# Kernel tuning notes

Measured on AMD Instinct MI355X. Metric: run time of the kernel, lower is better.

The kernel has to match this reference:

```python
import jax, jax.numpy as jnp
import numpy as np
from jax import lax

T, IN, H, B = 256, 2048, 2048, 8
K_INIT = 4.0

def setup_inputs() -> dict:
    key = jax.random.key(0)
    k1, k2, k3, k4, k5, k6 = jax.random.split(key, 6)
    k = 1.0 / np.sqrt(H)
    # simplex-init alphas: off-diagonal -K, diagonal log(1-(B-1)exp(-K)), plus small noise
    base = jnp.full((B, B), -K_INIT) + jnp.eye(B) * (np.log(1.0 - (B - 1) * np.exp(-K_INIT)) + K_INIT)
    alphas = base + 0.01 * jax.random.normal(k1, (B, B))
    return {
        "x": jax.random.normal(k2, (T, IN), dtype=jnp.float32),            # sentence of word vectors
        "W": jax.random.uniform(k3, (B, H, H), minval=-k, maxval=k),       # B recurrent basis matrices
        "alphas": alphas.astype(jnp.float32),                               # [B, B] mixing logits
        "bias": jax.random.uniform(k4, (H,), minval=-k, maxval=k),
        "v": jnp.eye(H, IN, dtype=jnp.float32),                             # input projection (init = eye)
        "fc_w": jax.random.uniform(k5, (H, H), minval=-k, maxval=k),
        "fc_b": jax.random.uniform(k6, (H,), minval=-k, maxval=k),
        "alpha_int": 0,
    }

def reference(x, W, alphas, bias, v, fc_w, fc_b, alpha_int):
    # normalise_alpha == softmax over the selected alpha row (simplex=True)
    alpha = jax.nn.softmax(alphas[alpha_int])                 # [B]
    u = jnp.einsum('b,bij->ij', alpha, W)                     # mixed recurrent weight [H, H]
    igates = x @ v.T                                          # all input gates at once [T, H]

    def step(h, ig):                                          # Elman cell: h = tanh(v@w + u@h + bias)
        h = jnp.tanh(ig + u @ h + bias)
        return h, None

    h0 = jnp.zeros((H,), dtype=x.dtype)
    h, _ = lax.scan(step, h0, igates)                         # sequential over T words
    out = jax.nn.sigmoid(h @ fc_w.T + fc_b)                   # fc(hidden.t()) then sigmoid
    return out[None, :]                                       # [1, H]
```

## Files before the change

kernel.cpp:

```cpp
#include <hip/hip_runtime.h>
#include <math.h>

#define HDIM    2048
#define TSTEPS  256
#define BBASIS  8
#define RING_D  4
#define NR      8

typedef float f32x4 __attribute__((ext_vector_type(4)));

__device__ inline void store_coherent_f4(float* p, f32x4 v) {
    asm volatile("global_store_dwordx4 %0, %1, off sc0 sc1"
                 :: "v"(p), "v"(v) : "memory");
}
__device__ inline f32x4 load_coherent_f4(const float* p) {
    f32x4 a;
    asm volatile("global_load_dwordx4 %0, %1, off sc0 sc1\n\t"
                 "s_waitcnt vmcnt(0)"
                 : "=&v"(a) : "v"(p) : "memory");
    return a;
}

__global__ __launch_bounds__(256, 1)
void prep_kernel(const float* __restrict__ x,
                 const float* __restrict__ W,
                 const float* __restrict__ alphas,
                 const float* __restrict__ v,
                 const int*   __restrict__ alpha_int,
                 float*       __restrict__ u_g,
                 float*       __restrict__ ig_g)
{
    const int tid  = threadIdx.x;
    const int bid  = blockIdx.x;
    const int wave = tid >> 6;
    const int lane = tid & 63;
    const int r0   = bid * 8 + wave * 2;

    __shared__ __align__(16) float x_tile[8][HDIM];

    const int ai = alpha_int[0];
    float a[BBASIS];
    float mx = -1e30f;
    #pragma unroll
    for (int b = 0; b < BBASIS; ++b) { a[b] = alphas[ai * BBASIS + b]; mx = fmaxf(mx, a[b]); }
    float ssum = 0.f;
    #pragma unroll
    for (int b = 0; b < BBASIS; ++b) { a[b] = expf(a[b] - mx); ssum += a[b]; }
    const float inv_s = 1.f / ssum;

    {
        float acc[2][8][4];
        #pragma unroll
        for (int q = 0; q < 2; ++q)
            #pragma unroll
            for (int k = 0; k < 8; ++k)
                #pragma unroll
                for (int i = 0; i < 4; ++i) acc[q][k][i] = 0.f;

        for (int b = 0; b < BBASIS; ++b) {
            const float ab = a[b] * inv_s;
            #pragma unroll
            for (int q = 0; q < 2; ++q) {
                const f32x4* wrow = (const f32x4*)(W + ((size_t)b * HDIM + (size_t)(r0 + q)) * HDIM);
                #pragma unroll
                for (int k = 0; k < 8; ++k) {
                    f32x4 w4 = wrow[lane + 64 * k];
                    acc[q][k][0] += ab * w4.x;
                    acc[q][k][1] += ab * w4.y;
                    acc[q][k][2] += ab * w4.z;
                    acc[q][k][3] += ab * w4.w;
                }
            }
        }
        #pragma unroll
        for (int q = 0; q < 2; ++q) {
            f32x4* urow = (f32x4*)(u_g + (size_t)(r0 + q) * HDIM);
            #pragma unroll
            for (int k = 0; k < 8; ++k) {
                f32x4 w4;
                w4.x = acc[q][k][0]; w4.y = acc[q][k][1];
                w4.z = acc[q][k][2]; w4.w = acc[q][k][3];
                urow[lane + 64 * k] = w4;
            }
        }
    }

    {
        float vr[2][8][4];
        #pragma unroll
        for (int q = 0; q < 2; ++q) {
            const f32x4* vrow = (const f32x4*)(v + (size_t)(r0 + q) * HDIM);
            #pragma unroll
            for (int k = 0; k < 8; ++k) {
                f32x4 t4 = vrow[lane + 64 * k];
                vr[q][k][0] = t4.x; vr[q][k][1] = t4.y; vr[q][k][2] = t4.z; vr[q][k][3] = t4.w;
            }
        }
        for (int tb = 0; tb < TSTEPS; tb += 8) {
            #pragma unroll
            for (int j = 0; j < 8; ++j) {
                const f32x4* xt4 = (const f32x4*)(x + (size_t)(tb + j) * HDIM);
                #pragma unroll
                for (int c = 0; c < 2; ++c)
                    ((f32x4*)x_tile[j])[tid + 256 * c] = xt4[tid + 256 * c];
            }
            __syncthreads();
            #pragma unroll
            for (int j = 0; j < 8; ++j) {
                float acc0 = 0.f, acc1 = 0.f;
                #pragma unroll
                for (int k = 0; k < 8; ++k) {
                    const f32x4 x4 = ((const f32x4*)x_tile[j])[lane + 64 * k];
                    acc0 += vr[0][k][0]*x4.x + vr[0][k][1]*x4.y + vr[0][k][2]*x4.z + vr[0][k][3]*x4.w;
                    acc1 += vr[1][k][0]*x4.x + vr[1][k][1]*x4.y + vr[1][k][2]*x4.z + vr[1][k][3]*x4.w;
                }
                #pragma unroll
                for (int off = 32; off > 0; off >>= 1) {
                    acc0 += __shfl_xor(acc0, off, 64);
                    acc1 += __shfl_xor(acc1, off, 64);
                }
                if (lane == 0)
                    *(float2*)&ig_g[(size_t)(tb + j) * HDIM + r0] = make_float2(acc0, acc1);
            }
            __syncthreads();
        }
    }
}

__global__ __launch_bounds__(512, 2)
void scan_kernel(const float* __restrict__ bias,
                 const float* __restrict__ fc_w,
                 const float* __restrict__ fc_b,
                 float*       __restrict__ out,
                 const float* __restrict__ u_g,
                 const float* __restrict__ ig_g,
                 float*       __restrict__ ring)
{
    const int tid  = threadIdx.x;
    const int bid  = blockIdx.x;
    const int wave = tid >> 6;
    const int lane = tid & 63;
    const int r0   = bid * 32 + wave * 4;

    __shared__ __align__(16) float h_lds[2][HDIM];
    __shared__ __align__(16) float ig_lds[TSTEPS][32];

    #pragma unroll
    for (int i = 0; i < 4; ++i) {
        const int c  = tid + 512 * i;
        const int t  = c >> 3;
        const int ch = c & 7;
        f32x4 g = *(const f32x4*)&ig_g[(size_t)t * HDIM + bid * 32 + ch * 4];
        *(f32x4*)&ig_lds[t][ch * 4] = g;
    }

    f32x4 U[4][8];
    #pragma unroll
    for (int q = 0; q < 4; ++q) {
        const float* urow = u_g + (size_t)(r0 + q) * HDIM;
        #pragma unroll
        for (int k = 0; k < 8; ++k) {
            asm volatile("global_load_dwordx4 %0, %1, off"
                         : "=&v"(U[q][k])
                         : "v"(urow + (size_t)(lane + 64 * k) * 4));
        }
    }
    asm volatile("s_waitcnt vmcnt(0)" ::: "memory");
    __builtin_amdgcn_sched_barrier(0);

    float bias4[4];
    #pragma unroll
    for (int q = 0; q < 4; ++q) bias4[q] = bias[r0 + q];

    h_lds[0][tid]        = 0.f;
    h_lds[0][tid + 512]  = 0.f;
    h_lds[0][tid + 1024] = 0.f;
    h_lds[0][tid + 1536] = 0.f;
    __syncthreads();

    int cur = 0;
    for (int t = 0; t < TSTEPS; ++t) {
        float acc0 = 0.f, acc1 = 0.f, acc2 = 0.f, acc3 = 0.f;
        #pragma unroll
        for (int k = 0; k < 8; ++k) {
            const f32x4 h4 = ((const f32x4*)h_lds[cur])[lane + 64 * k];
            acc0 += U[0][k].x*h4.x + U[0][k].y*h4.y + U[0][k].z*h4.z + U[0][k].w*h4.w;
            acc1 += U[1][k].x*h4.x + U[1][k].y*h4.y + U[1][k].z*h4.z + U[1][k].w*h4.w;
            acc2 += U[2][k].x*h4.x + U[2][k].y*h4.y + U[2][k].z*h4.z + U[2][k].w*h4.w;
            acc3 += U[3][k].x*h4.x + U[3][k].y*h4.y + U[3][k].z*h4.z + U[3][k].w*h4.w;
        }
        #pragma unroll
        for (int off = 32; off > 0; off >>= 1) {
            acc0 += __shfl_xor(acc0, off, 64);
            acc1 += __shfl_xor(acc1, off, 64);
            acc2 += __shfl_xor(acc2, off, 64);
            acc3 += __shfl_xor(acc3, off, 64);
        }
        const int   st     = t + 1;
        const float bias_f = ((st >> 2) & 1) ? 8.0f : -8.0f;
        float* slotbase = ring + (size_t)((st & (RING_D - 1)) * NR) * HDIM;

        const f32x4 ig4 = *(const f32x4*)&ig_lds[t][wave * 4];
        f32x4 hv;
        hv.x = tanhf(acc0 + ig4.x + bias4[0]) + bias_f;
        hv.y = tanhf(acc1 + ig4.y + bias4[1]) + bias_f;
        hv.z = tanhf(acc2 + ig4.z + bias4[2]) + bias_f;
        hv.w = tanhf(acc3 + ig4.w + bias4[3]) + bias_f;
        if (lane < NR)
            store_coherent_f4(slotbase + (size_t)lane * HDIM + r0, hv);

        const float* pp = slotbase + (size_t)(bid & (NR - 1)) * HDIM + 4 * tid;
        f32x4 hq = load_coherent_f4(pp);
        if (bias_f > 0.0f) {
            while (!((hq.x > 6.5f) & (hq.y > 6.5f) & (hq.z > 6.5f) & (hq.w > 6.5f))) {
                __builtin_amdgcn_s_sleep(1);
                hq = load_coherent_f4(pp);
            }
        } else {
            while (!((hq.x < -6.5f) & (hq.y < -6.5f) & (hq.z < -6.5f) & (hq.w < -6.5f))) {
                __builtin_amdgcn_s_sleep(1);
                hq = load_coherent_f4(pp);
            }
        }
        hq.x -= bias_f; hq.y -= bias_f; hq.z -= bias_f; hq.w -= bias_f;

        const int nxt = cur ^ 1;
        *(f32x4*)&h_lds[nxt][4 * tid] = hq;
        __syncthreads();
        cur = nxt;
    }

    {
        float acc0 = 0.f, acc1 = 0.f, acc2 = 0.f, acc3 = 0.f;
        const f32x4* f0 = (const f32x4*)(fc_w + (size_t)(r0 + 0) * HDIM);
        const f32x4* f1 = (const f32x4*)(fc_w + (size_t)(r0 + 1) * HDIM);
        const f32x4* f2 = (const f32x4*)(fc_w + (size_t)(r0 + 2) * HDIM);
        const f32x4* f3 = (const f32x4*)(fc_w + (size_t)(r0 + 3) * HDIM);
        #pragma unroll
        for (int k = 0; k < 8; ++k) {
            const f32x4 h4 = ((const f32x4*)h_lds[cur])[lane + 64 * k];
            f32x4 w0 = f0[lane + 64 * k];
            f32x4 w1 = f1[lane + 64 * k];
            f32x4 w2 = f2[lane + 64 * k];
            f32x4 w3 = f3[lane + 64 * k];
            acc0 += w0.x*h4.x + w0.y*h4.y + w0.z*h4.z + w0.w*h4.w;
            acc1 += w1.x*h4.x + w1.y*h4.y + w1.z*h4.z + w1.w*h4.w;
            acc2 += w2.x*h4.x + w2.y*h4.y + w2.z*h4.z + w2.w*h4.w;
            acc3 += w3.x*h4.x + w3.y*h4.y + w3.z*h4.z + w3.w*h4.w;
        }
        #pragma unroll
        for (int off = 32; off > 0; off >>= 1) {
            acc0 += __shfl_xor(acc0, off, 64);
            acc1 += __shfl_xor(acc1, off, 64);
            acc2 += __shfl_xor(acc2, off, 64);
            acc3 += __shfl_xor(acc3, off, 64);
        }
        if (lane == 0) {
            f32x4 o4;
            o4.x = 1.f / (1.f + expf(-(acc0 + fc_b[r0 + 0])));
            o4.y = 1.f / (1.f + expf(-(acc1 + fc_b[r0 + 1])));
            o4.z = 1.f / (1.f + expf(-(acc2 + fc_b[r0 + 2])));
            o4.w = 1.f / (1.f + expf(-(acc3 + fc_b[r0 + 3])));
            *(f32x4*)&out[r0] = o4;
        }
    }
}

__global__ __launch_bounds__(512, 1)
void elman_scan_self(const float* __restrict__ x,
                     const float* __restrict__ W,
                     const float* __restrict__ alphas,
                     const float* __restrict__ bias,
                     const float* __restrict__ v,
                     const float* __restrict__ fc_w,
                     const float* __restrict__ fc_b,
                     const int*   __restrict__ alpha_int,
                     float*       __restrict__ out,
                     float*       __restrict__ hbuf)
{
    const int tid  = threadIdx.x;
    const int bid  = blockIdx.x;
    const int wave = tid >> 6;
    const int lane = tid & 63;
    const int r0   = bid * 32 + wave * 4;

    __shared__ __align__(16) float x_tile[8][HDIM];
    __shared__ __align__(16) float ig_lds[TSTEPS][32];
    __shared__ __align__(16) float h_lds[2][HDIM];

    const int ai = alpha_int[0];
    float a[BBASIS];
    float mx = -1e30f;
    #pragma unroll
    for (int b = 0; b < BBASIS; ++b) { a[b] = alphas[ai * BBASIS + b]; mx = fmaxf(mx, a[b]); }
    float ssum = 0.f;
    #pragma unroll
    for (int b = 0; b < BBASIS; ++b) { a[b] = expf(a[b] - mx); ssum += a[b]; }
    const float inv_s = 1.f / ssum;

    {
        float vr[4][8][4];
        #pragma unroll
        for (int q = 0; q < 4; ++q) {
            const f32x4* vrow = (const f32x4*)(v + (size_t)(r0 + q) * HDIM);
            #pragma unroll
            for (int k = 0; k < 8; ++k) {
                f32x4 t4 = vrow[lane + 64 * k];
                vr[q][k][0] = t4.x; vr[q][k][1] = t4.y; vr[q][k][2] = t4.z; vr[q][k][3] = t4.w;
            }
        }
        for (int tb = 0; tb < TSTEPS; tb += 8) {
            #pragma unroll
            for (int j = 0; j < 8; ++j)
                *(f32x4*)&x_tile[j][4 * tid] =
                    *(const f32x4*)&x[(size_t)(tb + j) * HDIM + 4 * tid];
            __syncthreads();
            #pragma unroll
            for (int j = 0; j < 8; ++j) {
                float acc0 = 0.f, acc1 = 0.f, acc2 = 0.f, acc3 = 0.f;
                #pragma unroll
                for (int k = 0; k < 8; ++k) {
                    const f32x4 x4 = ((const f32x4*)x_tile[j])[lane + 64 * k];
                    acc0 += vr[0][k][0]*x4.x + vr[0][k][1]*x4.y + vr[0][k][2]*x4.z + vr[0][k][3]*x4.w;
                    acc1 += vr[1][k][0]*x4.x + vr[1][k][1]*x4.y + vr[1][k][2]*x4.z + vr[1][k][3]*x4.w;
                    acc2 += vr[2][k][0]*x4.x + vr[2][k][1]*x4.y + vr[2][k][2]*x4.z + vr[2][k][3]*x4.w;
                    acc3 += vr[3][k][0]*x4.x + vr[3][k][1]*x4.y + vr[3][k][2]*x4.z + vr[3][k][3]*x4.w;
                }
                #pragma unroll
                for (int off = 32; off > 0; off >>= 1) {
                    acc0 += __shfl_xor(acc0, off, 64);
                    acc1 += __shfl_xor(acc1, off, 64);
                    acc2 += __shfl_xor(acc2, off, 64);
                    acc3 += __shfl_xor(acc3, off, 64);
                }
                if (lane == 0) {
                    f32x4 ig4; ig4.x = acc0; ig4.y = acc1; ig4.z = acc2; ig4.w = acc3;
                    *(f32x4*)&ig_lds[tb + j][wave * 4] = ig4;
                }
            }
            __syncthreads();
        }
    }

    float u_reg[4][8][4];
    #pragma unroll
    for (int q = 0; q < 4; ++q)
        #pragma unroll
        for (int k = 0; k < 8; ++k)
            #pragma unroll
            for (int i = 0; i < 4; ++i) u_reg[q][k][i] = 0.f;

    for (int b = 0; b < BBASIS; ++b) {
        const float ab = a[b] * inv_s;
        #pragma unroll
        for (int q = 0; q < 4; ++q) {
            const f32x4* wrow = (const f32x4*)(W + ((size_t)b * HDIM + (size_t)(r0 + q)) * HDIM);
            #pragma unroll
            for (int k = 0; k < 8; ++k) {
                f32x4 w4 = wrow[lane + 64 * k];
                u_reg[q][k][0] += ab * w4.x;
                u_reg[q][k][1] += ab * w4.y;
                u_reg[q][k][2] += ab * w4.z;
                u_reg[q][k][3] += ab * w4.w;
            }
        }
    }
    float bias4[4];
    #pragma unroll
    for (int q = 0; q < 4; ++q) bias4[q] = bias[r0 + q];

    h_lds[0][tid] = 0.f; h_lds[0][tid + 512] = 0.f;
    h_lds[0][tid + 1024] = 0.f; h_lds[0][tid + 1536] = 0.f;
    __syncthreads();

    int cur = 0;
    for (int t = 0; t < TSTEPS; ++t) {
        float acc0 = 0.f, acc1 = 0.f, acc2 = 0.f, acc3 = 0.f;
        #pragma unroll
        for (int k = 0; k < 8; ++k) {
            const f32x4 h4 = ((const f32x4*)h_lds[cur])[lane + 64 * k];
            acc0 += u_reg[0][k][0]*h4.x + u_reg[0][k][1]*h4.y + u_reg[0][k][2]*h4.z + u_reg[0][k][3]*h4.w;
            acc1 += u_reg[1][k][0]*h4.x + u_reg[1][k][1]*h4.y + u_reg[1][k][2]*h4.z + u_reg[1][k][3]*h4.w;
            acc2 += u_reg[2][k][0]*h4.x + u_reg[2][k][1]*h4.y + u_reg[2][k][2]*h4.z + u_reg[2][k][3]*h4.w;
            acc3 += u_reg[3][k][0]*h4.x + u_reg[3][k][1]*h4.y + u_reg[3][k][2]*h4.z + u_reg[3][k][3]*h4.w;
        }
        #pragma unroll
        for (int off = 32; off > 0; off >>= 1) {
            acc0 += __shfl_xor(acc0, off, 64);
            acc1 += __shfl_xor(acc1, off, 64);
            acc2 += __shfl_xor(acc2, off, 64);
            acc3 += __shfl_xor(acc3, off, 64);
        }
        float* hg = hbuf + (size_t)(t + 1) * HDIM;
        if (lane == 0) {
            const f32x4 ig4 = *(const f32x4*)&ig_lds[t][wave * 4];
            f32x4 hv;
            hv.x = tanhf(acc0 + ig4.x + bias4[0]);
            hv.y = tanhf(acc1 + ig4.y + bias4[1]);
            hv.z = tanhf(acc2 + ig4.z + bias4[2]);
            hv.w = tanhf(acc3 + ig4.w + bias4[3]);
            store_coherent_f4(hg + r0, hv);
        }
        const float* pp = hg + 4 * tid;
        f32x4 hq = load_coherent_f4(pp);
        const unsigned s = 0xFFFFFFFFu;
        while ((__float_as_uint(hq.x) == s) | (__float_as_uint(hq.y) == s) |
               (__float_as_uint(hq.z) == s) | (__float_as_uint(hq.w) == s)) {
            __builtin_amdgcn_s_sleep(1);
            hq = load_coherent_f4(pp);
        }
        const int nxt = cur ^ 1;
        *(f32x4*)&h_lds[nxt][4 * tid] = hq;
        __syncthreads();
        cur = nxt;
    }

    {
        float acc0 = 0.f, acc1 = 0.f, acc2 = 0.f, acc3 = 0.f;
        const f32x4* f0 = (const f32x4*)(fc_w + (size_t)(r0 + 0) * HDIM);
        const f32x4* f1 = (const f32x4*)(fc_w + (size_t)(r0 + 1) * HDIM);
        const f32x4* f2 = (const f32x4*)(fc_w + (size_t)(r0 + 2) * HDIM);
        const f32x4* f3 = (const f32x4*)(fc_w + (size_t)(r0 + 3) * HDIM);
        #pragma unroll
        for (int k = 0; k < 8; ++k) {
            const f32x4 h4 = ((const f32x4*)h_lds[cur])[lane + 64 * k];
            f32x4 w0 = f0[lane + 64 * k];
            f32x4 w1 = f1[lane + 64 * k];
            f32x4 w2 = f2[lane + 64 * k];
            f32x4 w3 = f3[lane + 64 * k];
            acc0 += w0.x*h4.x + w0.y*h4.y + w0.z*h4.z + w0.w*h4.w;
            acc1 += w1.x*h4.x + w1.y*h4.y + w1.z*h4.z + w1.w*h4.w;
            acc2 += w2.x*h4.x + w2.y*h4.y + w2.z*h4.z + w2.w*h4.w;
            acc3 += w3.x*h4.x + w3.y*h4.y + w3.z*h4.z + w3.w*h4.w;
        }
        #pragma unroll
        for (int off = 32; off > 0; off >>= 1) {
            acc0 += __shfl_xor(acc0, off, 64);
            acc1 += __shfl_xor(acc1, off, 64);
            acc2 += __shfl_xor(acc2, off, 64);
            acc3 += __shfl_xor(acc3, off, 64);
        }
        if (lane == 0) {
            f32x4 o4;
            o4.x = 1.f / (1.f + expf(-(acc0 + fc_b[r0 + 0])));
            o4.y = 1.f / (1.f + expf(-(acc1 + fc_b[r0 + 1])));
            o4.z = 1.f / (1.f + expf(-(acc2 + fc_b[r0 + 2])));
            o4.w = 1.f / (1.f + expf(-(acc3 + fc_b[r0 + 3])));
            *(f32x4*)&out[r0] = o4;
        }
    }
}

extern "C" void kernel_launch(void* const* d_in, const int* in_sizes, int n_in,
                              void* d_out, int out_size, void* d_ws, size_t ws_size,
                              hipStream_t stream)
{
    const float* x      = (const float*)d_in[0];
    const float* W      = (const float*)d_in[1];
    const float* alphas = (const float*)d_in[2];
    const float* bias   = (const float*)d_in[3];
    const float* v      = (const float*)d_in[4];
    const float* fc_w   = (const float*)d_in[5];
    const float* fc_b   = (const float*)d_in[6];
    const int*   ai     = (const int*)d_in[7];
    float* out = (float*)d_out;

    const size_t RING_BYTES = (size_t)RING_D * NR * HDIM * sizeof(float);
    const size_t IG_OFF     = 0x80000;
    const size_t U_OFF      = IG_OFF + 0x200000;
    const size_t U_BYTES    = (size_t)HDIM * HDIM * sizeof(float);
    const size_t NEED       = U_OFF + U_BYTES;

    if (ws_size >= NEED) {
        float* ring = (float*)d_ws;
        float* ig_g = (float*)((char*)d_ws + IG_OFF);
        float* u_g  = (float*)((char*)d_ws + U_OFF);
        hipMemsetAsync(d_ws, 0, RING_BYTES, stream);
        prep_kernel<<<256, 256, 0, stream>>>(x, W, alphas, v, ai, u_g, ig_g);
        scan_kernel<<<64, 512, 0, stream>>>(bias, fc_w, fc_b, out, u_g, ig_g, (float*)ring);
    } else {
        float* hbuf = (float*)d_ws;
        const size_t hbuf_bytes = (size_t)(TSTEPS + 1) * HDIM * sizeof(float);
        hipMemsetAsync(d_ws, 0xFF, hbuf_bytes, stream);
        elman_scan_self<<<64, 512, 0, stream>>>(x, W, alphas, bias, v, fc_w, fc_b,
                                                ai, out, hbuf);
    }
}
```

Before: 993.9 us.

## Use single shared ring slot with atomic publishes and pipelined polling

Drops the 8-way replicated ring, so each block publishes its 4 hidden values once, as two 64-bit atomic exchanges into a single shared slot per step. All 64 blocks then poll the same slot. Polling uses two overlapping in-flight loads instead of load, wait and sleep, and the matvec runs at raised wave priority. This cuts publish traffic and polling latency on the per-step critical path, at the risk of more contention on one copy of the hidden state.

```diff
diff --git a/kernel.cpp b/kernel.cpp
--- a/kernel.cpp
+++ b/kernel.cpp
@@ -5,7 +5,6 @@
 #define TSTEPS  256
 #define BBASIS  8
 #define RING_D  4
-#define NR      8
 
 typedef float f32x4 __attribute__((ext_vector_type(4)));
 
@@ -180,6 +179,7 @@
 
     int cur = 0;
     for (int t = 0; t < TSTEPS; ++t) {
+        __builtin_amdgcn_s_setprio(1);
         float acc0 = 0.f, acc1 = 0.f, acc2 = 0.f, acc3 = 0.f;
         #pragma unroll
         for (int k = 0; k < 8; ++k) {
@@ -196,9 +196,12 @@
             acc2 += __shfl_xor(acc2, off, 64);
             acc3 += __shfl_xor(acc3, off, 64);
         }
+        __builtin_amdgcn_s_setprio(0);
+
         const int   st     = t + 1;
-        const float bias_f = ((st >> 2) & 1) ? 8.0f : -8.0f;
-        float* slotbase = ring + (size_t)((st & (RING_D - 1)) * NR) * HDIM;
+        const bool  bpos   = ((st >> 2) & 1) != 0;
+        const float bias_f = bpos ? 8.0f : -8.0f;
+        float* slotbase = ring + (size_t)(st & (RING_D - 1)) * HDIM;
 
         const f32x4 ig4 = *(const f32x4*)&ig_lds[t][wave * 4];
         f32x4 hv;
@@ -206,21 +209,41 @@
         hv.y = tanhf(acc1 + ig4.y + bias4[1]) + bias_f;
         hv.z = tanhf(acc2 + ig4.z + bias4[2]) + bias_f;
         hv.w = tanhf(acc3 + ig4.w + bias4[3]) + bias_f;
-        if (lane < NR)
-            store_coherent_f4(slotbase + (size_t)lane * HDIM + r0, hv);
-
-        const float* pp = slotbase + (size_t)(bid & (NR - 1)) * HDIM + 4 * tid;
-        f32x4 hq = load_coherent_f4(pp);
-        if (bias_f > 0.0f) {
-            while (!((hq.x > 6.5f) & (hq.y > 6.5f) & (hq.z > 6.5f) & (hq.w > 6.5f))) {
-                __builtin_amdgcn_s_sleep(1);
-                hq = load_coherent_f4(pp);
-            }
-        } else {
-            while (!((hq.x < -6.5f) & (hq.y < -6.5f) & (hq.z < -6.5f) & (hq.w < -6.5f))) {
-                __builtin_amdgcn_s_sleep(1);
-                hq = load_coherent_f4(pp);
-            }
+
+        if (lane < 2) {
+            const float lo = (lane == 0) ? hv.x : hv.z;
+            const float hi = (lane == 0) ? hv.y : hv.w;
+            unsigned long long bits =
+                ((unsigned long long)__float_as_uint(hi) << 32) | __float_as_uint(lo);
+            unsigned long long* dst = (unsigned long long*)(slotbase + r0) + lane;
+            (void)__hip_atomic_exchange(dst, bits, __ATOMIC_RELAXED,
+                                        __HIP_MEMORY_SCOPE_AGENT);
+        }
+
+        const float* pp = slotbase + 4 * tid;
+        f32x4 hq;
+        {
+            f32x4 A, B;
+            asm volatile("global_load_dwordx4 %0, %1, off sc0 sc1"
+                         : "=&v"(A) : "v"(pp) : "memory");
+            for (;;) {
+                asm volatile("global_load_dwordx4 %0, %1, off sc0 sc1"
+                             : "=&v"(B) : "v"(pp) : "memory");
+                asm volatile("s_waitcnt vmcnt(1)" ::: "memory");
+                __builtin_amdgcn_sched_barrier(0);
+                bool okA = bpos ? ((A.x >  6.5f) & (A.y >  6.5f) & (A.z >  6.5f) & (A.w >  6.5f))
+                                : ((A.x < -6.5f) & (A.y < -6.5f) & (A.z < -6.5f) & (A.w < -6.5f));
+                if (okA) { hq = A; break; }
+                asm volatile("global_load_dwordx4 %0, %1, off sc0 sc1"
+                             : "=&v"(A) : "v"(pp) : "memory");
+                asm volatile("s_waitcnt vmcnt(1)" ::: "memory");
+                __builtin_amdgcn_sched_barrier(0);
+                bool okB = bpos ? ((B.x >  6.5f) & (B.y >  6.5f) & (B.z >  6.5f) & (B.w >  6.5f))
+                                : ((B.x < -6.5f) & (B.y < -6.5f) & (B.z < -6.5f) & (B.w < -6.5f));
+                if (okB) { hq = B; break; }
+            }
+            asm volatile("s_waitcnt vmcnt(0)" ::: "memory");
+            __builtin_amdgcn_sched_barrier(0);
         }
         hq.x -= bias_f; hq.y -= bias_f; hq.z -= bias_f; hq.w -= bias_f;
 
@@ -465,7 +488,7 @@
     const int*   ai     = (const int*)d_in[7];
     float* out = (float*)d_out;
 
-    const size_t RING_BYTES = (size_t)RING_D * NR * HDIM * sizeof(float);
+    const size_t RING_BYTES = (size_t)RING_D * HDIM * sizeof(float);
     const size_t IG_OFF     = 0x80000;
     const size_t U_OFF      = IG_OFF + 0x200000;
     const size_t U_BYTES    = (size_t)HDIM * HDIM * sizeof(float);
```

Measured after the change: 1.213 ms. +22.1%, slower.

## Run the scan on a single XCC with L2-scoped sync and bf16 recurrent weights

Applied to the files above, without the earlier changes.

Stores the mixed recurrent matrix U as bf16 so each block can hold 8 rows in registers. A new scan kernel elects 32 blocks that all sit on one XCC using hardware XCC IDs and atomics. Those blocks exchange h through L2-scoped (sc0) loads and stores instead of system-coherent ones, which is meant to cut per-step sync latency across XCDs. If the election or spin waits time out, a flag falls back to the old 64-block cross-XCC scan. This adds bf16 rounding error in U and depends on 32 co-resident blocks landing on one XCC.

```diff
diff --git a/kernel.cpp b/kernel.cpp
--- a/kernel.cpp
+++ b/kernel.cpp
@@ -5,10 +5,25 @@
 #define TSTEPS  256
 #define BBASIS  8
 #define RING_D  4
+#define GRP     32
 #define NR      8
-
-typedef float f32x4 __attribute__((ext_vector_type(4)));
-
+#define FCAP    3000u
+#define PCAP    4096u
+
+typedef float    f32x4 __attribute__((ext_vector_type(4)));
+typedef unsigned u32x2 __attribute__((ext_vector_type(2)));
+
+__device__ inline void store_l2_f4(float* p, f32x4 v) {
+    asm volatile("global_store_dwordx4 %0, %1, off sc0"
+                 :: "v"(p), "v"(v) : "memory");
+}
+__device__ inline f32x4 load_l2_f4(const float* p) {
+    f32x4 a;
+    asm volatile("global_load_dwordx4 %0, %1, off sc0\n\t"
+                 "s_waitcnt vmcnt(0)"
+                 : "=&v"(a) : "v"(p) : "memory");
+    return a;
+}
 __device__ inline void store_coherent_f4(float* p, f32x4 v) {
     asm volatile("global_store_dwordx4 %0, %1, off sc0 sc1"
                  :: "v"(p), "v"(v) : "memory");
@@ -21,13 +36,18 @@
     return a;
 }
 
+__device__ inline unsigned bf16rne(float f) {
+    unsigned b = __float_as_uint(f);
+    return (b + 0x7FFFu + ((b >> 16) & 1u)) >> 16;
+}
+
 __global__ __launch_bounds__(256, 1)
 void prep_kernel(const float* __restrict__ x,
                  const float* __restrict__ W,
                  const float* __restrict__ alphas,
                  const float* __restrict__ v,
                  const int*   __restrict__ alpha_int,
-                 float*       __restrict__ u_g,
+                 unsigned*    __restrict__ ub_g,
                  float*       __restrict__ ig_g)
 {
     const int tid  = threadIdx.x;
@@ -74,13 +94,13 @@
         }
         #pragma unroll
         for (int q = 0; q < 2; ++q) {
-            f32x4* urow = (f32x4*)(u_g + (size_t)(r0 + q) * HDIM);
+            unsigned* ubrow = ub_g + (size_t)(r0 + q) * 1024;
             #pragma unroll
             for (int k = 0; k < 8; ++k) {
-                f32x4 w4;
-                w4.x = acc[q][k][0]; w4.y = acc[q][k][1];
-                w4.z = acc[q][k][2]; w4.w = acc[q][k][3];
-                urow[lane + 64 * k] = w4;
+                u32x2 p;
+                p.x = bf16rne(acc[q][k][0]) | (bf16rne(acc[q][k][1]) << 16);
+                p.y = bf16rne(acc[q][k][2]) | (bf16rne(acc[q][k][3]) << 16);
+                *(u32x2*)(ubrow + 128 * k + 2 * lane) = p;
             }
         }
     }
@@ -132,9 +152,211 @@
                  const float* __restrict__ fc_w,
                  const float* __restrict__ fc_b,
                  float*       __restrict__ out,
-                 const float* __restrict__ u_g,
+                 const unsigned* __restrict__ ub_g,
                  const float* __restrict__ ig_g,
+                 unsigned*    __restrict__ ctrl,
                  float*       __restrict__ ring)
+{
+    const int tid  = threadIdx.x;
+    const int wave = tid >> 6;
+    const int lane = tid & 63;
+
+    __shared__ int s_part, s_chunk;
+    __shared__ volatile int s_abort;
+    if (tid == 0) {
+        s_abort = 0;
+        unsigned xcc;
+        asm volatile("s_getreg_b32 %0, hwreg(HW_REG_XCC_ID)" : "=s"(xcc));
+        xcc &= 7u;
+        unsigned tk = __hip_atomic_fetch_add(&ctrl[xcc], 1u,
+                                             __ATOMIC_RELAXED, __HIP_MEMORY_SCOPE_AGENT);
+        if (tk == GRP - 1) {
+            unsigned exp = 0u;
+            __hip_atomic_compare_exchange_strong(&ctrl[8], &exp, xcc + 1u,
+                                                 __ATOMIC_RELAXED, __ATOMIC_RELAXED,
+                                                 __HIP_MEMORY_SCOPE_AGENT);
+        }
+        unsigned w = 0, it = 0; int ok = 1;
+        for (;;) {
+            w = __hip_atomic_load(&ctrl[8], __ATOMIC_RELAXED, __HIP_MEMORY_SCOPE_AGENT);
+            if (w) break;
+            ++it;
+            if (it >= FCAP ||
+                ((it & 15u) == 0u &&
+                 __hip_atomic_load(&ctrl[9], __ATOMIC_RELAXED, __HIP_MEMORY_SCOPE_AGENT))) {
+                ok = 0; break;
+            }
+            __builtin_amdgcn_s_sleep(8);
+        }
+        if (!ok) {
+            __hip_atomic_store(&ctrl[9], 1u, __ATOMIC_RELAXED, __HIP_MEMORY_SCOPE_AGENT);
+            s_part = 0; s_chunk = 0;
+        } else {
+            s_part  = (w - 1u == xcc) && (tk < (unsigned)GRP);
+            s_chunk = (int)tk;
+        }
+    }
+    __syncthreads();
+    if (!s_part) return;
+    const int chunk = s_chunk;
+    const int r0    = chunk * 64 + wave * 8;
+
+    __shared__ __align__(16) float h_lds[2][HDIM];
+    __shared__ __align__(16) float ig_lds[TSTEPS][64];
+
+    #pragma unroll
+    for (int i = 0; i < 8; ++i) {
+        const int c  = tid + 512 * i;
+        const int t  = c >> 4;
+        const int ch = c & 15;
+        f32x4 g = *(const f32x4*)&ig_g[(size_t)t * HDIM + chunk * 64 + ch * 4];
+        *(f32x4*)&ig_lds[t][ch * 4] = g;
+    }
+
+    u32x2 Ub[8][8];
+    #pragma unroll
+    for (int q = 0; q < 8; ++q) {
+        const unsigned* ubrow = ub_g + (size_t)(r0 + q) * 1024;
+        #pragma unroll
+        for (int k = 0; k < 8; ++k) {
+            asm volatile("global_load_dwordx2 %0, %1, off"
+                         : "=&v"(Ub[q][k])
+                         : "v"(ubrow + 128 * k + 2 * lane));
+        }
+    }
+    asm volatile("s_waitcnt vmcnt(0)" ::: "memory");
+    __builtin_amdgcn_sched_barrier(0);
+
+    float bias8[8];
+    #pragma unroll
+    for (int q = 0; q < 8; ++q) bias8[q] = bias[r0 + q];
+
+    h_lds[0][tid]        = 0.f;
+    h_lds[0][tid + 512]  = 0.f;
+    h_lds[0][tid + 1024] = 0.f;
+    h_lds[0][tid + 1536] = 0.f;
+    __syncthreads();
+
+    int cur = 0;
+    for (int t = 0; t < TSTEPS; ++t) {
+        float acc[8];
+        #pragma unroll
+        for (int q = 0; q < 8; ++q) acc[q] = 0.f;
+        #pragma unroll
+        for (int k = 0; k < 8; ++k) {
+            const f32x4 h4 = ((const f32x4*)h_lds[cur])[lane + 64 * k];
+            #pragma unroll
+            for (int q = 0; q < 8; ++q) {
+                const u32x2 up = Ub[q][k];
+                const float u0 = __uint_as_float(up.x << 16);
+                const float u1 = __uint_as_float(up.x & 0xFFFF0000u);
+                const float u2 = __uint_as_float(up.y << 16);
+                const float u3 = __uint_as_float(up.y & 0xFFFF0000u);
+                acc[q] += u0*h4.x + u1*h4.y + u2*h4.z + u3*h4.w;
+            }
+        }
+        #pragma unroll
+        for (int off = 32; off > 0; off >>= 1)
+            #pragma unroll
+            for (int q = 0; q < 8; ++q)
+                acc[q] += __shfl_xor(acc[q], off, 64);
+
+        const int   st     = t + 1;
+        const bool  bpos   = ((st >> 2) & 1) != 0;
+        const float bias_f = bpos ? 8.0f : -8.0f;
+        float* slotbase = ring + (size_t)(st & (RING_D - 1)) * HDIM;
+
+        float hval[8];
+        #pragma unroll
+        for (int q = 0; q < 8; ++q) {
+            const float ig = ig_lds[t][wave * 8 + q];
+            hval[q] = tanhf(acc[q] + ig + bias8[q]) + bias_f;
+        }
+        if (lane < 2) {
+            f32x4 hv;
+            if (lane == 0) { hv.x = hval[0]; hv.y = hval[1]; hv.z = hval[2]; hv.w = hval[3]; }
+            else           { hv.x = hval[4]; hv.y = hval[5]; hv.z = hval[6]; hv.w = hval[7]; }
+            store_l2_f4(slotbase + r0 + 4 * lane, hv);
+        }
+
+        const float* pp = slotbase + 4 * tid;
+        f32x4 hq;
+        {
+            unsigned it = 0; int fail = 0;
+            for (;;) {
+                hq = load_l2_f4(pp);
+                bool ok = bpos ? ((hq.x >  6.5f) & (hq.y >  6.5f) & (hq.z >  6.5f) & (hq.w >  6.5f))
+                               : ((hq.x < -6.5f) & (hq.y < -6.5f) & (hq.z < -6.5f) & (hq.w < -6.5f));
+                if (ok) break;
+                ++it;
+                if (s_abort) { fail = 1; break; }
+                if ((it & 63u) == 0u) {
+                    if (it >= PCAP ||
+                        __hip_atomic_load(&ctrl[9], __ATOMIC_RELAXED, __HIP_MEMORY_SCOPE_AGENT)) {
+                        fail = 1; break;
+                    }
+                }
+                __builtin_amdgcn_s_sleep(1);
+            }
+            if (fail) s_abort = 1;
+        }
+        const int nxt = cur ^ 1;
+        hq.x -= bias_f; hq.y -= bias_f; hq.z -= bias_f; hq.w -= bias_f;
+        *(f32x4*)&h_lds[nxt][4 * tid] = hq;
+        __syncthreads();
+        if (s_abort) {
+            if (tid == 0)
+                __hip_atomic_store(&ctrl[9], 1u, __ATOMIC_RELAXED, __HIP_MEMORY_SCOPE_AGENT);
+            return;
+        }
+        cur = nxt;
+    }
+
+    {
+        float acc[8];
+        #pragma unroll
+        for (int q = 0; q < 8; ++q) acc[q] = 0.f;
+        #pragma unroll
+        for (int k = 0; k < 8; ++k) {
+            const f32x4 h4 = ((const f32x4*)h_lds[cur])[lane + 64 * k];
+            #pragma unroll
+            for (int q = 0; q < 8; ++q) {
+                const f32x4 w4 = ((const f32x4*)(fc_w + (size_t)(r0 + q) * HDIM))[lane + 64 * k];
+                acc[q] += w4.x*h4.x + w4.y*h4.y + w4.z*h4.z + w4.w*h4.w;
+            }
+        }
+        #pragma unroll
+        for (int off = 32; off > 0; off >>= 1)
+            #pragma unroll
+            for (int q = 0; q < 8; ++q)
+                acc[q] += __shfl_xor(acc[q], off, 64);
+        if (lane < 2) {
+            f32x4 o4;
+            #pragma unroll
+            for (int j = 0; j < 4; ++j) {
+                const int q = lane * 4 + j;
+                const float s = 1.f / (1.f + expf(-(acc[q] + fc_b[r0 + q])));
+                if (j == 0) o4.x = s; else if (j == 1) o4.y = s;
+                else if (j == 2) o4.z = s; else o4.w = s;
+            }
+            *(f32x4*)&out[r0 + 4 * lane] = o4;
+        }
+    }
+    asm volatile("s_waitcnt vmcnt(0)" ::: "memory");
+    __syncthreads();
+    if (tid == 0)
+        __hip_atomic_fetch_add(&ctrl[10], 1u, __ATOMIC_RELAXED, __HIP_MEMORY_SCOPE_AGENT);
+}
+
+__global__ __launch_bounds__(512, 2)
+void scan_fb_kernel(const float* __restrict__ bias,
+                    const float* __restrict__ fc_w,
+                    const float* __restrict__ fc_b,
+                    float*       __restrict__ out,
+                    const unsigned* __restrict__ ub_g,
+                    const float* __restrict__ ig_g,
+                    unsigned*    __restrict__ ctrl,
+                    float*       __restrict__ ring)
 {
     const int tid  = threadIdx.x;
     const int bid  = blockIdx.x;
@@ -142,6 +364,12 @@
     const int lane = tid & 63;
     const int r0   = bid * 32 + wave * 4;
 
+    __shared__ unsigned s_done;
+    if (tid == 0)
+        s_done = __hip_atomic_load(&ctrl[10], __ATOMIC_RELAXED, __HIP_MEMORY_SCOPE_AGENT);
+    __syncthreads();
+    if (s_done == (unsigned)GRP) return;
+
     __shared__ __align__(16) float h_lds[2][HDIM];
     __shared__ __align__(16) float ig_lds[TSTEPS][32];
 
@@ -154,15 +382,15 @@
         *(f32x4*)&ig_lds[t][ch * 4] = g;
     }
 
-    f32x4 U[4][8];
+    u32x2 Ub[4][8];
     #pragma unroll
     for (int q = 0; q < 4; ++q) {
-        const float* urow = u_g + (size_t)(r0 + q) * HDIM;
+        const unsigned* ubrow = ub_g + (size_t)(r0 + q) * 1024;
         #pragma unroll
         for (int k = 0; k < 8; ++k) {
-            asm volatile("global_load_dwordx4 %0, %1, off"
-                         : "=&v"(U[q][k])
-                         : "v"(urow + (size_t)(lane + 64 * k) * 4));
+            asm volatile("global_load_dwordx2 %0, %1, off"
+                         : "=&v"(Ub[q][k])
+                         : "v"(ubrow + 128 * k + 2 * lane));
         }
     }
     asm volatile("s_waitcnt vmcnt(0)" ::: "memory");
@@ -180,38 +408,48 @@
 
     int cur = 0;
     for (int t = 0; t < TSTEPS; ++t) {
-        float acc0 = 0.f, acc1 = 0.f, acc2 = 0.f, acc3 = 0.f;
+        float acc[4];
+        #pragma unroll
+        for (int q = 0; q < 4; ++q) acc[q] = 0.f;
         #pragma unroll
         for (int k = 0; k < 8; ++k) {
             const f32x4 h4 = ((const f32x4*)h_lds[cur])[lane + 64 * k];
-            acc0 += U[0][k].x*h4.x + U[0][k].y*h4.y + U[0][k].z*h4.z + U[0][k].w*h4.w;
-            acc1 += U[1][k].x*h4.x + U[1][k].y*h4.y + U[1][k].z*h4.z + U[1][k].w*h4.w;
-            acc2 += U[2][k].x*h4.x + U[2][k].y*h4.y + U[2][k].z*h4.z + U[2][k].w*h4.w;
-            acc3 += U[3][k].x*h4.x + U[3][k].y*h4.y + U[3][k].z*h4.z + U[3][k].w*h4.w;
-        }
-        #pragma unroll
-        for (int off = 32; off > 0; off >>= 1) {
-            acc0 += __shfl_xor(acc0, off, 64);
-            acc1 += __shfl_xor(acc1, off, 64);
-            acc2 += __shfl_xor(acc2, off, 64);
-            acc3 += __shfl_xor(acc3, off, 64);
-        }
+            #pragma unroll
+            for (int q = 0; q < 4; ++q) {
+                const u32x2 up = Ub[q][k];
+                const float u0 = __uint_as_float(up.x << 16);
+                const float u1 = __uint_as_float(up.x & 0xFFFF0000u);
+                const float u2 = __uint_as_float(up.y << 16);
+                const float u3 = __uint_as_float(up.y & 0xFFFF0000u);
+                acc[q] += u0*h4.x + u1*h4.y + u2*h4.z + u3*h4.w;
+            }
+        }
+        #pragma unroll
+        for (int off = 32; off > 0; off >>= 1)
+            #pragma unroll
+            for (int q = 0; q < 4; ++q)
+                acc[q] += __shfl_xor(acc[q], off, 64);
+
         const int   st     = t + 1;
-        const float bias_f = ((st >> 2) & 1) ? 8.0f : -8.0f;
+        const bool  bpos   = ((st >> 2) & 1) != 0;
+        const float bias_f = bpos ? 8.0f : -8.0f;
         float* slotbase = ring + (size_t)((st & (RING_D - 1)) * NR) * HDIM;
 
-        const f32x4 ig4 = *(const f32x4*)&ig_lds[t][wave * 4];
-        f32x4 hv;
-        hv.x = tanhf(acc0 + ig4.x + bias4[0]) + bias_f;
-        hv.y = tanhf(acc1 + ig4.y + bias4[1]) + bias_f;
-        hv.z = tanhf(acc2 + ig4.z + bias4[2]) + bias_f;
-        hv.w = tanhf(acc3 + ig4.w + bias4[3]) + bias_f;
-        if (lane < NR)
-            store_coherent_f4(slotbase + (size_t)lane * HDIM + r0, hv);
+        float hval[4];
+        #pragma unroll
+        for (int q = 0; q < 4; ++q) {
+            const float ig = ig_lds[t][wave * 4 + q];
+            hval[q] = tanhf(acc[q] + ig + bias4[q]) + bias_f;
+        }
+        {
+            f32x4 hv; hv.x = hval[0]; hv.y = hval[1]; hv.z = hval[2]; hv.w = hval[3];
+            if (lane < NR)
+                store_coherent_f4(slotbase + (size_t)lane * HDIM + r0, hv);
+        }
 
         const float* pp = slotbase + (size_t)(bid & (NR - 1)) * HDIM + 4 * tid;
         f32x4 hq = load_coherent_f4(pp);
-        if (bias_f > 0.0f) {
+        if (bpos) {
             while (!((hq.x > 6.5f) & (hq.y > 6.5f) & (hq.z > 6.5f) & (hq.w > 6.5f))) {
                 __builtin_amdgcn_s_sleep(1);
                 hq = load_coherent_f4(pp);
@@ -231,221 +469,29 @@
     }
 
     {
-        float acc0 = 0.f, acc1 = 0.f, acc2 = 0.f, acc3 = 0.f;
-        const f32x4* f0 = (const f32x4*)(fc_w + (size_t)(r0 + 0) * HDIM);
-        const f32x4* f1 = (const f32x4*)(fc_w + (size_t)(r0 + 1) * HDIM);
-        const f32x4* f2 = (const f32x4*)(fc_w + (size_t)(r0 + 2) * HDIM);
-        const f32x4* f3 = (const f32x4*)(fc_w + (size_t)(r0 + 3) * HDIM);
+        float acc[4];
+        #pragma unroll
+        for (int q = 0; q < 4; ++q) acc[q] = 0.f;
         #pragma unroll
         for (int k = 0; k < 8; ++k) {
             const f32x4 h4 = ((const f32x4*)h_lds[cur])[lane + 64 * k];
-            f32x4 w0 = f0[lane + 64 * k];
-            f32x4 w1 = f1[lane + 64 * k];
-            f32x4 w2 = f2[lane + 64 * k];
-            f32x4 w3 = f3[lane + 64 * k];
-            acc0 += w0.x*h4.x + w0.y*h4.y + w0.z*h4.z + w0.w*h4.w;
-            acc1 += w1.x*h4.x + w1.y*h4.y + w1.z*h4.z + w1.w*h4.w;
-            acc2 += w2.x*h4.x + w2.y*h4.y + w2.z*h4.z + w2.w*h4.w;
-            acc3 += w3.x*h4.x + w3.y*h4.y + w3.z*h4.z + w3.w*h4.w;
-        }
-        #pragma unroll
-        for (int off = 32; off > 0; off >>= 1) {
-            acc0 += __shfl_xor(acc0, off, 64);
-            acc1 += __shfl_xor(acc1, off, 64);
-            acc2 += __shfl_xor(acc2, off, 64);
-            acc3 += __shfl_xor(acc3, off, 64);
-        }
+            #pragma unroll
+            for (int q = 0; q < 4; ++q) {
+                const f32x4 w4 = ((const f32x4*)(fc_w + (size_t)(r0 + q) * HDIM))[lane + 64 * k];
+                acc[q] += w4.x*h4.x + w4.y*h4.y + w4.z*h4.z + w4.w*h4.w;
+            }
+        }
+        #pragma unroll
+        for (int off = 32; off > 0; off >>= 1)
+            #pragma unroll
+            for (int q = 0; q < 4; ++q)
+                acc[q] += __shfl_xor(acc[q], off, 64);
         if (lane == 0) {
             f32x4 o4;
-            o4.x = 1.f / (1.f + expf(-(acc0 + fc_b[r0 + 0])));
-            o4.y = 1.f / (1.f + expf(-(acc1 + fc_b[r0 + 1])));
-            o4.z = 1.f / (1.f + expf(-(acc2 + fc_b[r0 + 2])));
-            o4.w = 1.f / (1.f + expf(-(acc3 + fc_b[r0 + 3])));
-            *(f32x4*)&out[r0] = o4;
-        }
-    }
-}
-
-__global__ __launch_bounds__(512, 1)
-void elman_scan_self(const float* __restrict__ x,
-                     const float* __restrict__ W,
-                     const float* __restrict__ alphas,
-                     const float* __restrict__ bias,
-                     const float* __restrict__ v,
-                     const float* __restrict__ fc_w,
-                     const float* __restrict__ fc_b,
-                     const int*   __restrict__ alpha_int,
-                     float*       __restrict__ out,
-                     float*       __restrict__ hbuf)
-{
-    const int tid  = threadIdx.x;
-    const int bid  = blockIdx.x;
-    const int wave = tid >> 6;
-    const int lane = tid & 63;
-    const int r0   = bid * 32 + wave * 4;
-
-    __shared__ __align__(16) float x_tile[8][HDIM];
-    __shared__ __align__(16) float ig_lds[TSTEPS][32];
-    __shared__ __align__(16) float h_lds[2][HDIM];
-
-    const int ai = alpha_int[0];
-    float a[BBASIS];
-    float mx = -1e30f;
-    #pragma unroll
-    for (int b = 0; b < BBASIS; ++b) { a[b] = alphas[ai * BBASIS + b]; mx = fmaxf(mx, a[b]); }
-    float ssum = 0.f;
-    #pragma unroll
-    for (int b = 0; b < BBASIS; ++b) { a[b] = expf(a[b] - mx); ssum += a[b]; }
-    const float inv_s = 1.f / ssum;
-
-    {
-        float vr[4][8][4];
-        #pragma unroll
-        for (int q = 0; q < 4; ++q) {
-            const f32x4* vrow = (const f32x4*)(v + (size_t)(r0 + q) * HDIM);
-            #pragma unroll
-            for (int k = 0; k < 8; ++k) {
-                f32x4 t4 = vrow[lane + 64 * k];
-                vr[q][k][0] = t4.x; vr[q][k][1] = t4.y; vr[q][k][2] = t4.z; vr[q][k][3] = t4.w;
-            }
-        }
-        for (int tb = 0; tb < TSTEPS; tb += 8) {
-            #pragma unroll
-            for (int j = 0; j < 8; ++j)
-                *(f32x4*)&x_tile[j][4 * tid] =
-                    *(const f32x4*)&x[(size_t)(tb + j) * HDIM + 4 * tid];
-            __syncthreads();
-            #pragma unroll
-            for (int j = 0; j < 8; ++j) {
-                float acc0 = 0.f, acc1 = 0.f, acc2 = 0.f, acc3 = 0.f;
-                #pragma unroll
-                for (int k = 0; k < 8; ++k) {
-                    const f32x4 x4 = ((const f32x4*)x_tile[j])[lane + 64 * k];
-                    acc0 += vr[0][k][0]*x4.x + vr[0][k][1]*x4.y + vr[0][k][2]*x4.z + vr[0][k][3]*x4.w;
-                    acc1 += vr[1][k][0]*x4.x + vr[1][k][1]*x4.y + vr[1][k][2]*x4.z + vr[1][k][3]*x4.w;
-                    acc2 += vr[2][k][0]*x4.x + vr[2][k][1]*x4.y + vr[2][k][2]*x4.z + vr[2][k][3]*x4.w;
-                    acc3 += vr[3][k][0]*x4.x + vr[3][k][1]*x4.y + vr[3][k][2]*x4.z + vr[3][k][3]*x4.w;
-                }
-                #pragma unroll
-                for (int off = 32; off > 0; off >>= 1) {
-                    acc0 += __shfl_xor(acc0, off, 64);
-                    acc1 += __shfl_xor(acc1, off, 64);
-                    acc2 += __shfl_xor(acc2, off, 64);
-                    acc3 += __shfl_xor(acc3, off, 64);
-                }
-                if (lane == 0) {
-                    f32x4 ig4; ig4.x = acc0; ig4.y = acc1; ig4.z = acc2; ig4.w = acc3;
-                    *(f32x4*)&ig_lds[tb + j][wave * 4] = ig4;
-                }
-            }
-            __syncthreads();
-        }
-    }
-
-    float u_reg[4][8][4];
-    #pragma unroll
-    for (int q = 0; q < 4; ++q)
-        #pragma unroll
-        for (int k = 0; k < 8; ++k)
-            #pragma unroll
-            for (int i = 0; i < 4; ++i) u_reg[q][k][i] = 0.f;
-
-    for (int b = 0; b < BBASIS; ++b) {
-        const float ab = a[b] * inv_s;
-        #pragma unroll
-        for (int q = 0; q < 4; ++q) {
-            const f32x4* wrow = (const f32x4*)(W + ((size_t)b * HDIM + (size_t)(r0 + q)) * HDIM);
-            #pragma unroll
-            for (int k = 0; k < 8; ++k) {
-                f32x4 w4 = wrow[lane + 64 * k];
-                u_reg[q][k][0] += ab * w4.x;
-                u_reg[q][k][1] += ab * w4.y;
-                u_reg[q][k][2] += ab * w4.z;
-                u_reg[q][k][3] += ab * w4.w;
-            }
-        }
-    }
-    float bias4[4];
-    #pragma unroll
-    for (int q = 0; q < 4; ++q) bias4[q] = bias[r0 + q];
-
-    h_lds[0][tid] = 0.f; h_lds[0][tid + 512] = 0.f;
-    h_lds[0][tid + 1024] = 0.f; h_lds[0][tid + 1536] = 0.f;
-    __syncthreads();
-
-    int cur = 0;
-    for (int t = 0; t < TSTEPS; ++t) {
-        float acc0 = 0.f, acc1 = 0.f, acc2 = 0.f, acc3 = 0.f;
-        #pragma unroll
-        for (int k = 0; k < 8; ++k) {
-            const f32x4 h4 = ((const f32x4*)h_lds[cur])[lane + 64 * k];
-            acc0 += u_reg[0][k][0]*h4.x + u_reg[0][k][1]*h4.y + u_reg[0][k][2]*h4.z + u_reg[0][k][3]*h4.w;
-            acc1 += u_reg[1][k][0]*h4.x + u_reg[1][k][1]*h4.y + u_reg[1][k][2]*h4.z + u_reg[1][k][3]*h4.w;
-            acc2 += u_reg[2][k][0]*h4.x + u_reg[2][k][1]*h4.y + u_reg[2][k][2]*h4.z + u_reg[2][k][3]*h4.w;
-            acc3 += u_reg[3][k][0]*h4.x + u_reg[3][k][1]*h4.y + u_reg[3][k][2]*h4.z + u_reg[3][k][3]*h4.w;
-        }
-        #pragma unroll
-        for (int off = 32; off > 0; off >>= 1) {
-            acc0 += __shfl_xor(acc0, off, 64);
-            acc1 += __shfl_xor(acc1, off, 64);
-            acc2 += __shfl_xor(acc2, off, 64);
-            acc3 += __shfl_xor(acc3, off, 64);
-        }
-        float* hg = hbuf + (size_t)(t + 1) * HDIM;
-        if (lane == 0) {
-            const f32x4 ig4 = *(const f32x4*)&ig_lds[t][wave * 4];
-            f32x4 hv;
-            hv.x = tanhf(acc0 + ig4.x + bias4[0]);
-            hv.y = tanhf(acc1 + ig4.y + bias4[1]);
-            hv.z = tanhf(acc2 + ig4.z + bias4[2]);
-            hv.w = tanhf(acc3 + ig4.w + bias4[3]);
-            store_coherent_f4(hg + r0, hv);
-        }
-        const float* pp = hg + 4 * tid;
-        f32x4 hq = load_coherent_f4(pp);
-        const unsigned s = 0xFFFFFFFFu;
-        while ((__float_as_uint(hq.x) == s) | (__float_as_uint(hq.y) == s) |
-               (__float_as_uint(hq.z) == s) | (__float_as_uint(hq.w) == s)) {
-            __builtin_amdgcn_s_sleep(1);
-            hq = load_coherent_f4(pp);
-        }
-        const int nxt = cur ^ 1;
-        *(f32x4*)&h_lds[nxt][4 * tid] = hq;
-        __syncthreads();
-        cur = nxt;
-    }
-
-    {
-        float acc0 = 0.f, acc1 = 0.f, acc2 = 0.f, acc3 = 0.f;
-        const f32x4* f0 = (const f32x4*)(fc_w + (size_t)(r0 + 0) * HDIM);
-        const f32x4* f1 = (const f32x4*)(fc_w + (size_t)(r0 + 1) * HDIM);
-        const f32x4* f2 = (const f32x4*)(fc_w + (size_t)(r0 + 2) * HDIM);
-        const f32x4* f3 = (const f32x4*)(fc_w + (size_t)(r0 + 3) * HDIM);
-        #pragma unroll
-        for (int k = 0; k < 8; ++k) {
-            const f32x4 h4 = ((const f32x4*)h_lds[cur])[lane + 64 * k];
-            f32x4 w0 = f0[lane + 64 * k];
-            f32x4 w1 = f1[lane + 64 * k];
-            f32x4 w2 = f2[lane + 64 * k];
-            f32x4 w3 = f3[lane + 64 * k];
-            acc0 += w0.x*h4.x + w0.y*h4.y + w0.z*h4.z + w0.w*h4.w;
-            acc1 += w1.x*h4.x + w1.y*h4.y + w1.z*h4.z + w1.w*h4.w;
-            acc2 += w2.x*h4.x + w2.y*h4.y + w2.z*h4.z + w2.w*h4.w;
-            acc3 += w3.x*h4.x + w3.y*h4.y + w3.z*h4.z + w3.w*h4.w;
-        }
-        #pragma unroll
-        for (int off = 32; off > 0; off >>= 1) {
-            acc0 += __shfl_xor(acc0, off, 64);
-            acc1 += __shfl_xor(acc1, off, 64);
-            acc2 += __shfl_xor(acc2, off, 64);
-            acc3 += __shfl_xor(acc3, off, 64);
-        }
-        if (lane == 0) {
-            f32x4 o4;
-            o4.x = 1.f / (1.f + expf(-(acc0 + fc_b[r0 + 0])));
-            o4.y = 1.f / (1.f + expf(-(acc1 + fc_b[r0 + 1])));
-            o4.z = 1.f / (1.f + expf(-(acc2 + fc_b[r0 + 2])));
-            o4.w = 1.f / (1.f + expf(-(acc3 + fc_b[r0 + 3])));
+            o4.x = 1.f / (1.f + expf(-(acc[0] + fc_b[r0 + 0])));
+            o4.y = 1.f / (1.f + expf(-(acc[1] + fc_b[r0 + 1])));
+            o4.z = 1.f / (1.f + expf(-(acc[2] + fc_b[r0 + 2])));
+            o4.w = 1.f / (1.f + expf(-(acc[3] + fc_b[r0 + 3])));
             *(f32x4*)&out[r0] = o4;
         }
     }
@@ -465,24 +511,30 @@
     const int*   ai     = (const int*)d_in[7];
     float* out = (float*)d_out;
 
-    const size_t RING_BYTES = (size_t)RING_D * NR * HDIM * sizeof(float);
-    const size_t IG_OFF     = 0x80000;
-    const size_t U_OFF      = IG_OFF + 0x200000;
-    const size_t U_BYTES    = (size_t)HDIM * HDIM * sizeof(float);
-    const size_t NEED       = U_OFF + U_BYTES;
+    const size_t RINGA_OFF = 4096;
+    const size_t RINGB_OFF = 0x10000;
+    const size_t IG_OFF    = 0x80000;
+    const size_t UB_OFF    = IG_OFF + 0x200000;
+    const size_t UB_BYTES  = (size_t)HDIM * 1024 * sizeof(unsigned);
+    const size_t NEED      = UB_OFF + UB_BYTES;
 
     if (ws_size >= NEED) {
-        float* ring = (float*)d_ws;
-        float* ig_g = (float*)((char*)d_ws + IG_OFF);
-        float* u_g  = (float*)((char*)d_ws + U_OFF);
-        hipMemsetAsync(d_ws, 0, RING_BYTES, stream);
-        prep_kernel<<<256, 256, 0, stream>>>(x, W, alphas, v, ai, u_g, ig_g);
-        scan_kernel<<<64, 512, 0, stream>>>(bias, fc_w, fc_b, out, u_g, ig_g, (float*)ring);
+        unsigned* ctrl  = (unsigned*)d_ws;
+        float*    ringA = (float*)((char*)d_ws + RINGA_OFF);
+        float*    ringB = (float*)((char*)d_ws + RINGB_OFF);
+        float*    ig_g  = (float*)((char*)d_ws + IG_OFF);
+        unsigned* ub_g  = (unsigned*)((char*)d_ws + UB_OFF);
+        hipMemsetAsync(d_ws, 0, RINGB_OFF + (size_t)RING_D * NR * HDIM * sizeof(float), stream);
+        prep_kernel<<<256, 256, 0, stream>>>(x, W, alphas, v, ai, ub_g, ig_g);
+        scan_kernel<<<256, 512, 0, stream>>>(bias, fc_w, fc_b, out, ub_g, ig_g, ctrl, ringA);
+        scan_fb_kernel<<<64, 512, 0, stream>>>(bias, fc_w, fc_b, out, ub_g, ig_g, ctrl, ringB);
     } else {
-        float* hbuf = (float*)d_ws;
-        const size_t hbuf_bytes = (size_t)(TSTEPS + 1) * HDIM * sizeof(float);
-        hipMemsetAsync(d_ws, 0xFF, hbuf_bytes, stream);
-        elman_scan_self<<<64, 512, 0, stream>>>(x, W, alphas, bias, v, fc_w, fc_b,
-                                                ai, out, hbuf);
-    }
-}
+        unsigned* ctrl  = (unsigned*)d_ws;
+        float*    ringB = (float*)((char*)d_ws + RINGA_OFF);
+        float*    ig_g  = (float*)((char*)d_ws + RINGA_OFF + 0x40000);
+        unsigned* ub_g  = (unsigned*)((char*)d_ws + RINGA_OFF + 0x240000);
+        hipMemsetAsync(d_ws, 0, RINGA_OFF + (size_t)RING_D * NR * HDIM * sizeof(float), stream);
+        prep_kernel<<<256, 256, 0, stream>>>(x, W, alphas, v, ai, ub_g, ig_g);
+        scan_fb_kernel<<<64, 512, 0, stream>>>(bias, fc_w, fc_b, out, ub_g, ig_g, ctrl, ringB);
+    }
+}
```

Measured after the change: 2.038 ms. +105.0%, slower.
